# Optimization experiments

Hardware: AMD Instinct MI355X
Metric: run time of the kernel (lower is better)

## Reference

```python
import jax, jax.numpy as jnp
import numpy as np

B, S, D, H, DK = 2, 2048, 1024, 16, 64
NUM_BUCKETS, MAX_DIST = 32, 128
EPS = 1e-6


def _relative_position_bucket(rel, num_buckets=NUM_BUCKETS, max_distance=MAX_DIST):
    # bidirectional (T5 encoder) bucketing
    nb = num_buckets // 2
    bucket = (rel > 0).astype(jnp.int32) * nb
    n = jnp.abs(rel)
    max_exact = nb // 2
    is_small = n < max_exact
    large = max_exact + (
        jnp.log(jnp.maximum(n, 1).astype(jnp.float32) / max_exact)
        / np.log(max_distance / max_exact)
        * (nb - max_exact)
    ).astype(jnp.int32)
    large = jnp.minimum(large, nb - 1)
    return bucket + jnp.where(is_small, n, large)


def softmax1(logits):
    # off-by-one softmax: exp(x-m) / (sum(exp(x-m)) + exp(-m))
    m = jax.lax.stop_gradient(jnp.max(logits, axis=-1, keepdims=True))
    e = jnp.exp(logits - m)
    return e / (jnp.sum(e, axis=-1, keepdims=True) + jnp.exp(-m))


def setup_inputs() -> dict:
    key = jax.random.key(0)
    ks = jax.random.split(key, 8)
    scale = 0.02
    return {
        "hidden_states": jax.random.normal(ks[0], (B, S, D), dtype=jnp.float32),
        "delete_gate_mask": jax.random.normal(ks[1], (B, S, 1), dtype=jnp.float32),
        "ln_w": jnp.ones((D,), dtype=jnp.float32),
        "q_w": jax.random.normal(ks[2], (D, H * DK), dtype=jnp.float32) * scale,
        "k_w": jax.random.normal(ks[3], (D, H * DK), dtype=jnp.float32) * scale,
        "v_w": jax.random.normal(ks[4], (D, H * DK), dtype=jnp.float32) * scale,
        "o_w": jax.random.normal(ks[5], (H * DK, D), dtype=jnp.float32) * scale,
        "rel_emb": jax.random.normal(ks[6], (NUM_BUCKETS, H), dtype=jnp.float32) * scale,
    }


def reference(hidden_states, delete_gate_mask, ln_w, q_w, k_w, v_w, o_w, rel_emb):
    # T5LayerNorm (RMS norm, no mean subtraction, no bias)
    var = jnp.mean(jnp.square(hidden_states), axis=-1, keepdims=True)
    x = hidden_states * jax.lax.rsqrt(var + EPS) * ln_w

    # projections (T5 Linear layers have no bias, no 1/sqrt(d) scaling)
    q = (x @ q_w).reshape(B, S, H, DK).transpose(0, 2, 1, 3)  # bhqd
    k = (x @ k_w).reshape(B, S, H, DK).transpose(0, 2, 1, 3)  # bhkd
    v = (x @ v_w).reshape(B, S, H, DK).transpose(0, 2, 1, 3)  # bhkd

    scores = jnp.einsum("bhqd,bhkd->bhqk", q, k)

    # relative position bias: [1, H, S, S]
    pos = jnp.arange(S)
    rel = pos[None, :] - pos[:, None]  # key_pos - query_pos
    bucket = _relative_position_bucket(rel)  # [S, S]
    position_bias = rel_emb[bucket].transpose(2, 0, 1)[None]  # [1,H,S,S]

    # delete gate: [B,S,1] -> additive mask over key axis [B,1,1,S]
    gate = delete_gate_mask[..., 0][:, None, None, :]

    scores = scores + position_bias + gate
    attn = softmax1(scores.astype(jnp.float32)).astype(scores.dtype)

    attn_out = jnp.einsum("bhqk,bhkd->bhqd", attn, v)
    attn_out = attn_out.transpose(0, 2, 1, 3).reshape(B, S, H * DK) @ o_w

    # residual (dropout disabled at p=0)
    return hidden_states + attn_out
```

## Files before the change

kernel.cpp:

```cpp
#include <hip/hip_runtime.h>
#include <hip/hip_bf16.h>
#include <math.h>

typedef __attribute__((ext_vector_type(8))) short short8;
typedef __attribute__((ext_vector_type(4))) float f32x4;

#define S_LEN   2048
#define DMODEL  1024
#define NHEAD   16
#define HDK     64
#define NBATCH  2
#define MTOT    (NBATCH*S_LEN)
#define LOG2E   1.4426950408889634f

__device__ __forceinline__ unsigned short f2bf(float f) {
  union { float f; unsigned u; } c; c.f = f;
  unsigned r = c.u + 0x7FFFu + ((c.u >> 16) & 1u);
  return (unsigned short)(r >> 16);
}

__device__ __forceinline__ short8 lds_ld16(const unsigned short* p) {
  return *reinterpret_cast<const short8*>(p);
}

__device__ __forceinline__ void gload_lds16(const unsigned short* g, unsigned short* l) {
  __builtin_amdgcn_global_load_lds(
      (const __attribute__((address_space(1))) unsigned int*)g,
      (__attribute__((address_space(3))) unsigned int*)l, 16, 0, 0);
}

__global__ __launch_bounds__(256) void transpose_w_kernel(
    const float* __restrict__ qw, const float* __restrict__ kw,
    const float* __restrict__ vw, const float* __restrict__ ow,
    unsigned short* __restrict__ wqkv, unsigned short* __restrict__ wo) {
  int z = blockIdx.z;
  const float* src = (z==0)?qw:(z==1)?kw:(z==2)?vw:ow;
  unsigned short* dst = (z<3) ? (wqkv + (size_t)z*DMODEL*DMODEL) : wo;
  __shared__ float tile[32][33];
  int n0 = blockIdx.x*32, k0 = blockIdx.y*32;
  int tx = threadIdx.x, ty = threadIdx.y;
  for (int r = ty; r < 32; r += 8)
    tile[r][tx] = src[(size_t)(k0+r)*DMODEL + n0 + tx];
  __syncthreads();
  for (int r = ty; r < 32; r += 8)
    dst[(size_t)(n0+r)*DMODEL + k0 + tx] = f2bf(tile[tx][r]);
}

__global__ void bias_table_kernel(const float* __restrict__ rel_emb,
                                  float* __restrict__ btab) {
  int idx = blockIdx.x*256 + threadIdx.x;
  if (idx >= NHEAD*4095) return;
  int h = idx / 4095, rp = idx % 4095, rel = rp - 2047;
  int bucket = (rel > 0) ? 16 : 0;
  int n = (rel < 0) ? -rel : rel;
  int v;
  if (n < 8) v = n;
  else {
    float lrv = logf((float)n * 0.125f) / 2.7725887f * 8.0f;
    v = 8 + (int)lrv;
    if (v > 15) v = 15;
  }
  btab[idx] = rel_emb[(size_t)(bucket + v)*NHEAD + h] * LOG2E;
}

__global__ __launch_bounds__(256) void rmsnorm_kernel(
    const float* __restrict__ hs, const float* __restrict__ lnw,
    unsigned short* __restrict__ xo) {
  int row = blockIdx.x, t = threadIdx.x;
  const float4 v = ((const float4*)(hs + (size_t)row*DMODEL))[t];
  float ss = v.x*v.x + v.y*v.y + v.z*v.z + v.w*v.w;
  #pragma unroll
  for (int off = 32; off >= 1; off >>= 1) ss += __shfl_xor(ss, off, 64);
  __shared__ float wsum[4];
  if ((t & 63) == 0) wsum[t >> 6] = ss;
  __syncthreads();
  float tot = wsum[0] + wsum[1] + wsum[2] + wsum[3];
  float sc = rsqrtf(tot * (1.0f/DMODEL) + 1e-6f);
  const float4 lw = ((const float4*)lnw)[t];
  uint2 o;
  o.x = (unsigned)f2bf(v.x*sc*lw.x) | ((unsigned)f2bf(v.y*sc*lw.y) << 16);
  o.y = (unsigned)f2bf(v.z*sc*lw.z) | ((unsigned)f2bf(v.w*sc*lw.w) << 16);
  ((uint2*)(xo + (size_t)row*DMODEL))[t] = o;
}

template<int EPI>
__global__ __launch_bounds__(256) void gemm128(
    const unsigned short* __restrict__ A,
    const unsigned short* __restrict__ Bt,
    unsigned short* __restrict__ Oq, unsigned short* __restrict__ Ok,
    unsigned short* __restrict__ Ov,
    const float* __restrict__ resid, float* __restrict__ Of) {
  __shared__ unsigned short As[128*64];
  __shared__ unsigned short Bs[128*64];
  const int m0 = blockIdx.x*128, n0 = blockIdx.y*128;
  const unsigned short* Bz = Bt + ((EPI==0) ? (size_t)blockIdx.z*DMODEL*DMODEL : 0);
  const int t = threadIdx.x, lane = t & 63, w = t >> 6;
  const int g = lane >> 4, lr = lane & 15;
  const int wr = (w >> 1)*64, wc = (w & 1)*64;

  f32x4 acc[4][4];
  #pragma unroll
  for (int mi = 0; mi < 4; mi++)
    #pragma unroll
    for (int ni = 0; ni < 4; ni++) acc[mi][ni] = (f32x4){0.f,0.f,0.f,0.f};

  const unsigned short* ag[4]; const unsigned short* bg[4];
  unsigned short* al[4]; unsigned short* bl[4];
  #pragma unroll
  for (int i = 0; i < 4; i++) {
    int slot = t + i*256, row = slot >> 3, c8 = slot & 7;
    int cs = c8 ^ (row & 7);
    ag[i] = A  + (size_t)(m0 + row)*DMODEL + cs*8;
    bg[i] = Bz + (size_t)(n0 + row)*DMODEL + cs*8;
    al[i] = As + slot*8;
    bl[i] = Bs + slot*8;
  }

  for (int kk = 0; kk < DMODEL; kk += 64) {
    #pragma unroll
    for (int i = 0; i < 4; i++) {
      gload_lds16(ag[i] + kk, al[i]);
      gload_lds16(bg[i] + kk, bl[i]);
    }
    __syncthreads();
    #pragma unroll
    for (int ks = 0; ks < 2; ks++) {
      short8 af[4], bfr[4];
      #pragma unroll
      for (int mi = 0; mi < 4; mi++) {
        int R = wr + mi*16 + lr;
        af[mi] = lds_ld16(As + R*64 + (((ks*4 + g) ^ (R & 7)) << 3));
      }
      #pragma unroll
      for (int ni = 0; ni < 4; ni++) {
        int R = wc + ni*16 + lr;
        bfr[ni] = lds_ld16(Bs + R*64 + (((ks*4 + g) ^ (R & 7)) << 3));
      }
      #pragma unroll
      for (int mi = 0; mi < 4; mi++)
        #pragma unroll
        for (int ni = 0; ni < 4; ni++)
          acc[mi][ni] = __builtin_amdgcn_mfma_f32_16x16x32_bf16(af[mi], bfr[ni], acc[mi][ni], 0, 0, 0);
    }
    __syncthreads();
  }

  if (EPI == 0) {
    unsigned short* dst = (blockIdx.z == 0) ? Oq : Ok;
    const float osc = (blockIdx.z == 0) ? LOG2E : 1.0f;
    #pragma unroll
    for (int mi = 0; mi < 4; mi++) {
      #pragma unroll
      for (int r = 0; r < 4; r++) {
        int m = m0 + wr + mi*16 + g*4 + r;
        int b = m >> 11, s = m & (S_LEN-1);
        unsigned short* drow = dst + ((size_t)b*NHEAD*S_LEN + s)*HDK;
        #pragma unroll
        for (int ni = 0; ni < 4; ni++) {
          int n = n0 + wc + ni*16 + lr;
          int h = n >> 6, dcol = n & 63;
          drow[(size_t)h*S_LEN*HDK + dcol] = f2bf(acc[mi][ni][r] * osc);
        }
      }
    }
  } else if (EPI == 2) {
    #pragma unroll
    for (int ni = 0; ni < 4; ni++) {
      int n = n0 + wc + ni*16 + lr;
      int b = n >> 11, s = n & (S_LEN-1);
      #pragma unroll
      for (int mi = 0; mi < 4; mi++)
        #pragma unroll
        for (int r = 0; r < 4; r++) {
          int m = m0 + wr + mi*16 + g*4 + r;
          Ov[((size_t)b*DMODEL + m)*S_LEN + s] = f2bf(acc[mi][ni][r]);
        }
    }
  } else {
    #pragma unroll
    for (int mi = 0; mi < 4; mi++) {
      #pragma unroll
      for (int r = 0; r < 4; r++) {
        int m = m0 + wr + mi*16 + g*4 + r;
        const float* rrow = resid + (size_t)m*DMODEL;
        float* orow = Of + (size_t)m*DMODEL;
        #pragma unroll
        for (int ni = 0; ni < 4; ni++) {
          int n = n0 + wc + ni*16 + lr;
          orow[n] = rrow[n] + acc[mi][ni][r];
        }
      }
    }
  }
}

__global__ __launch_bounds__(256, 2) void attn_kernel(
    const unsigned short* __restrict__ Qg,
    const unsigned short* __restrict__ Kg,
    const unsigned short* __restrict__ Vtg,
    const float* __restrict__ btab,
    const float* __restrict__ gmask,
    unsigned short* __restrict__ Og) {
  __shared__ __align__(16) unsigned short Kl[2][64][64];
  __shared__ __align__(16) unsigned short Vl[2][64][64];
  __shared__ __align__(16) unsigned short Pl[4][16*64];
  __shared__ __align__(16) float gl[S_LEN];

  const int flat = blockIdx.x;
  const int xcd = flat & 7, j = flat >> 3;
  const int bh = xcd*4 + (j >> 4), qx = j & 15;
  const int b = bh >> 4, h = bh & 15;
  const int q0 = qx * 128;

  const int t = threadIdx.x, w = t >> 6, lane = t & 63;
  const int g = lane >> 4, lr = lane & 15, l7 = lane & 7;
  const int srow0 = t >> 3, sg0 = t & 7, srow1 = srow0 + 32;
  const int swz = (sg0 ^ (srow0 & 7)) << 3;

  const unsigned short* Qb = Qg  + (size_t)bh*S_LEN*HDK;
  const unsigned short* Kb = Kg  + (size_t)bh*S_LEN*HDK;
  const unsigned short* Vb = Vtg + (size_t)bh*HDK*S_LEN;

  {
    const float4* gm4 = (const float4*)(gmask + (size_t)b*S_LEN);
    #pragma unroll
    for (int i = 0; i < 2; i++) {
      int idx = t + i*256;
      float4 gv = gm4[idx];
      float4 gs; gs.x = gv.x*LOG2E; gs.y = gv.y*LOG2E; gs.z = gv.z*LOG2E; gs.w = gv.w*LOG2E;
      ((float4*)gl)[idx] = gs;
    }
  }

  const int qs0A = q0 + w*32, qs0B = qs0A + 16;
  short8 qfA0 = *reinterpret_cast<const short8*>(Qb + (size_t)(qs0A+lr)*HDK + g*8);
  short8 qfA1 = *reinterpret_cast<const short8*>(Qb + (size_t)(qs0A+lr)*HDK + 32 + g*8);
  short8 qfB0 = *reinterpret_cast<const short8*>(Qb + (size_t)(qs0B+lr)*HDK + g*8);
  short8 qfB1 = *reinterpret_cast<const short8*>(Qb + (size_t)(qs0B+lr)*HDK + 32 + g*8);

  f32x4 accA[4], accB[4];
  #pragma unroll
  for (int n = 0; n < 4; n++) { accA[n] = (f32x4){0.f,0.f,0.f,0.f}; accB[n] = (f32x4){0.f,0.f,0.f,0.f}; }
  float mA = -1e30f, lA = 0.f, mB = -1e30f, lB = 0.f;

  const float* btb = btab + (size_t)h*4095 + 2047;
  const float cpos = btb[91];
  const float cneg = btb[-91];

  {
    *reinterpret_cast<uint4*>(&Kl[0][srow0][swz]) =
        *reinterpret_cast<const uint4*>(Kb + (size_t)srow0*HDK + sg0*8);
    *reinterpret_cast<uint4*>(&Kl[0][srow1][swz]) =
        *reinterpret_cast<const uint4*>(Kb + (size_t)srow1*HDK + sg0*8);
    *reinterpret_cast<uint4*>(&Vl[0][srow0][swz]) =
        *reinterpret_cast<const uint4*>(Vb + (size_t)srow0*S_LEN + sg0*8);
    *reinterpret_cast<uint4*>(&Vl[0][srow1][swz]) =
        *reinterpret_cast<const uint4*>(Vb + (size_t)srow1*S_LEN + sg0*8);
  }

  char* prow = (char*)&Pl[w][0] + lr*128;

  int cur = 0;
  const int NT = S_LEN/64;
  for (int kt = 0; kt < NT; ++kt) {
    const int key0 = kt*64;
    __syncthreads();

    uint4 nk0, nk1, nv0, nv1;
    const bool pf = (kt + 1 < NT);
    if (pf) {
      nk0 = *reinterpret_cast<const uint4*>(Kb + (size_t)(key0+64+srow0)*HDK + sg0*8);
      nk1 = *reinterpret_cast<const uint4*>(Kb + (size_t)(key0+64+srow1)*HDK + sg0*8);
      nv0 = *reinterpret_cast<const uint4*>(Vb + (size_t)srow0*S_LEN + key0+64 + sg0*8);
      nv1 = *reinterpret_cast<const uint4*>(Vb + (size_t)srow1*S_LEN + key0+64 + sg0*8);
    }

    short8 bk[4][2];
    #pragma unroll
    for (int n = 0; n < 4; n++) {
      const unsigned short* kr = &Kl[cur][n*16 + lr][0];
      bk[n][0] = lds_ld16(kr + ((g ^ l7) << 3));
      bk[n][1] = lds_ld16(kr + (((4 + g) ^ l7) << 3));
    }
    short8 bv[2][4];
    #pragma unroll
    for (int c = 0; c < 2; c++)
      #pragma unroll
      for (int n = 0; n < 4; n++)
        bv[c][n] = lds_ld16(&Vl[cur][n*16 + lr][((4*c + g) ^ l7) << 3]);
    float4 gq[4];
    #pragma unroll
    for (int n = 0; n < 4; n++) gq[n] = *(const float4*)&gl[key0 + n*16 + g*4];

    f32x4 svA[4], svB[4];
    __builtin_amdgcn_s_setprio(1);
    #pragma unroll
    for (int n = 0; n < 4; n++) {
      f32x4 z = (f32x4){0.f,0.f,0.f,0.f};
      svA[n] = __builtin_amdgcn_mfma_f32_16x16x32_bf16(bk[n][0], qfA0, z, 0, 0, 0);
      svA[n] = __builtin_amdgcn_mfma_f32_16x16x32_bf16(bk[n][1], qfA1, svA[n], 0, 0, 0);
      svB[n] = __builtin_amdgcn_mfma_f32_16x16x32_bf16(bk[n][0], qfB0, z, 0, 0, 0);
      svB[n] = __builtin_amdgcn_mfma_f32_16x16x32_bf16(bk[n][1], qfB1, svB[n], 0, 0, 0);
    }
    __builtin_amdgcn_s_setprio(0);

#define PROCESS_SET(sv_, m_, l_, acc_, qs0_)                                          \
    {                                                                                 \
      float s_[4][4];                                                                 \
      _Pragma("unroll") for (int n = 0; n < 4; n++)                                   \
        _Pragma("unroll") for (int r = 0; r < 4; r++) s_[n][r] = sv_[n][r];           \
      const int dband = key0 - (qs0_);                                                \
      if (dband > -154 && dband < 106) {                                              \
        const float* btq = btb + (dband - lr);                                        \
        _Pragma("unroll") for (int n = 0; n < 4; n++)                                 \
          _Pragma("unroll") for (int r = 0; r < 4; r++)                               \
            s_[n][r] += gq[n][r] + btq[n*16 + g*4 + r];                               \
      } else {                                                                        \
        const float cc = (dband > 0) ? cpos : cneg;                                   \
        _Pragma("unroll") for (int n = 0; n < 4; n++)                                 \
          _Pragma("unroll") for (int r = 0; r < 4; r++)                               \
            s_[n][r] += gq[n][r] + cc;                                                \
      }                                                                               \
      float pmax = s_[0][0];                                                          \
      _Pragma("unroll") for (int n = 0; n < 4; n++)                                   \
        _Pragma("unroll") for (int r = 0; r < 4; r++) pmax = fmaxf(pmax, s_[n][r]);   \
      if (__any(pmax > m_ + 8.0f)) {                                                  \
        float tm = pmax;                                                              \
        tm = fmaxf(tm, __shfl_xor(tm, 16));                                           \
        tm = fmaxf(tm, __shfl_xor(tm, 32));                                           \
        float mnew = fmaxf(m_, tm);                                                   \
        float scv = exp2f(m_ - mnew);                                                 \
        m_ = mnew; l_ *= scv;                                                         \
        _Pragma("unroll") for (int r = 0; r < 4; r++) {                               \
          float s4 = __shfl(scv, g*4 + r, 16);                                        \
          _Pragma("unroll") for (int n = 0; n < 4; n++) acc_[n][r] *= s4;             \
        }                                                                             \
      }                                                                               \
      _Pragma("unroll") for (int n = 0; n < 4; n++)                                   \
        _Pragma("unroll") for (int r = 0; r < 4; r++) {                               \
          float p = exp2f(s_[n][r] - m_);                                             \
          s_[n][r] = p; l_ += p;                                                      \
        }                                                                             \
      _Pragma("unroll") for (int n = 0; n < 4; n++) {                                 \
        unsigned plo_, phi_;                                                          \
        asm("v_cvt_pk_bf16_f32 %0, %1, %2" : "=v"(plo_) : "v"(s_[n][0]), "v"(s_[n][1])); \
        asm("v_cvt_pk_bf16_f32 %0, %1, %2" : "=v"(phi_) : "v"(s_[n][2]), "v"(s_[n][3])); \
        uint2 pw_; pw_.x = plo_; pw_.y = phi_;                                        \
        *reinterpret_cast<uint2*>(prow + ((((2*n + (g>>1)) ^ l7) << 4) + ((g & 1) << 3))) = pw_; \
      }                                                                               \
      __builtin_amdgcn_s_setprio(1);                                                  \
      _Pragma("unroll") for (int c = 0; c < 2; c++) {                                 \
        short8 pa_ = lds_ld16((const unsigned short*)(prow + (((4*c + g) ^ l7) << 4))); \
        _Pragma("unroll") for (int n = 0; n < 4; n++)                                 \
          acc_[n] = __builtin_amdgcn_mfma_f32_16x16x32_bf16(pa_, bv[c][n], acc_[n], 0, 0, 0); \
      }                                                                               \
      __builtin_amdgcn_s_setprio(0);                                                  \
    }

    PROCESS_SET(svA, mA, lA, accA, qs0A)
    PROCESS_SET(svB, mB, lB, accB, qs0B)
#undef PROCESS_SET

    if (pf) {
      *reinterpret_cast<uint4*>(&Kl[cur^1][srow0][swz]) = nk0;
      *reinterpret_cast<uint4*>(&Kl[cur^1][srow1][swz]) = nk1;
      *reinterpret_cast<uint4*>(&Vl[cur^1][srow0][swz]) = nv0;
      *reinterpret_cast<uint4*>(&Vl[cur^1][srow1][swz]) = nv1;
    }
    cur ^= 1;
  }

#define FINAL_SET(m_, l_, acc_, qs0_)                                                 \
  {                                                                                   \
    float rs = l_;                                                                    \
    rs += __shfl_xor(rs, 16);                                                         \
    rs += __shfl_xor(rs, 32);                                                         \
    float inv = 1.0f / (rs + exp2f(-m_));                                             \
    _Pragma("unroll") for (int r = 0; r < 4; r++) {                                   \
      float inv4 = __shfl(inv, g*4 + r, 16);                                          \
      int srw = (qs0_) + g*4 + r;                                                     \
      unsigned short* orow = Og + ((size_t)b*S_LEN + srw)*DMODEL + h*HDK;             \
      _Pragma("unroll") for (int n = 0; n < 4; n++)                                   \
        orow[n*16 + lr] = f2bf(acc_[n][r] * inv4);                                    \
    }                                                                                 \
  }
  FINAL_SET(mA, lA, accA, qs0A)
  FINAL_SET(mB, lB, accB, qs0B)
#undef FINAL_SET
}

extern "C" void kernel_launch(void* const* d_in, const int* in_sizes, int n_in,
                              void* d_out, int out_size, void* d_ws, size_t ws_size,
                              hipStream_t stream) {
  const float* hs   = (const float*)d_in[0];
  const float* gate = (const float*)d_in[1];
  const float* lnw  = (const float*)d_in[2];
  const float* qw   = (const float*)d_in[3];
  const float* kw   = (const float*)d_in[4];
  const float* vw   = (const float*)d_in[5];
  const float* ow   = (const float*)d_in[6];
  const float* rel  = (const float*)d_in[7];
  float* out = (float*)d_out;

  char* ws = (char*)d_ws;
  const size_t MB = 1ull << 20;
  unsigned short* xbf  = (unsigned short*)(ws);
  unsigned short* wqkv = (unsigned short*)(ws + 8*MB);
  unsigned short* wo   = (unsigned short*)(ws + 14*MB);
  unsigned short* qb   = (unsigned short*)(ws + 16*MB);
  unsigned short* kb   = (unsigned short*)(ws + 24*MB);
  unsigned short* vt   = (unsigned short*)(ws + 32*MB);
  unsigned short* ao   = (unsigned short*)(ws + 40*MB);
  float*          btab = (float*)(ws + 48*MB);

  transpose_w_kernel<<<dim3(32,32,4), dim3(32,8), 0, stream>>>(qw, kw, vw, ow, wqkv, wo);
  bias_table_kernel<<<dim3(256), dim3(256), 0, stream>>>(rel, btab);
  rmsnorm_kernel<<<dim3(MTOT), dim3(256), 0, stream>>>(hs, lnw, xbf);
  gemm128<0><<<dim3(MTOT/128, DMODEL/128, 2), dim3(256), 0, stream>>>(
      xbf, wqkv, qb, kb, nullptr, nullptr, nullptr);
  gemm128<2><<<dim3(DMODEL/128, MTOT/128, 1), dim3(256), 0, stream>>>(
      wqkv + (size_t)2*DMODEL*DMODEL, xbf, nullptr, nullptr, vt, nullptr, nullptr);
  attn_kernel<<<dim3(512), dim3(256), 0, stream>>>(
      qb, kb, vt, btab, gate, ao);
  gemm128<1><<<dim3(MTOT/128, DMODEL/128, 1), dim3(256), 0, stream>>>(
      ao, wo, nullptr, nullptr, nullptr, hs, out);
}
```

Before: 154.7 us.

## Drop online max in attention, fold gate into V, load K/V directly

The attention softmax no longer tracks a running max or rescales. The exp(gate) factor is pulled out of the logits and applied to V in the V-projection epilogue. The row sum is computed by an extra MFMA of P against a bf16 exp(gate) vector, and the final normaliser becomes 1/(sum+1). The constant bias is injected through the MFMA accumulator init. K/V LDS double-buffering and the block barrier are removed, so each wave reads K/V fragments straight from global memory. This cuts per-tile max reductions, shuffles and syncs, but risks overflow when logits are large and adds redundant global traffic across waves.

```diff
diff --git a/kernel.cpp b/kernel.cpp
--- a/kernel.cpp
+++ b/kernel.cpp
@@ -61,6 +61,15 @@
     if (v > 15) v = 15;
   }
   btab[idx] = rel_emb[(size_t)(bucket + v)*NHEAD + h] * LOG2E;
+}
+
+__global__ void eg_kernel(const float* __restrict__ gmask,
+                          float* __restrict__ egf,
+                          unsigned short* __restrict__ egb) {
+  int i = blockIdx.x*256 + threadIdx.x;
+  float e = __expf(gmask[i]);
+  egf[i] = e;
+  egb[i] = f2bf(e);
 }
 
 __global__ __launch_bounds__(256) void rmsnorm_kernel(
@@ -89,7 +98,8 @@
     const unsigned short* __restrict__ Bt,
     unsigned short* __restrict__ Oq, unsigned short* __restrict__ Ok,
     unsigned short* __restrict__ Ov,
-    const float* __restrict__ resid, float* __restrict__ Of) {
+    const float* __restrict__ resid, float* __restrict__ Of,
+    const float* __restrict__ escale) {
   __shared__ unsigned short As[128*64];
   __shared__ unsigned short Bs[128*64];
   const int m0 = blockIdx.x*128, n0 = blockIdx.y*128;
@@ -168,12 +178,13 @@
     for (int ni = 0; ni < 4; ni++) {
       int n = n0 + wc + ni*16 + lr;
       int b = n >> 11, s = n & (S_LEN-1);
+      float e = escale[n];
       #pragma unroll
       for (int mi = 0; mi < 4; mi++)
         #pragma unroll
         for (int r = 0; r < 4; r++) {
           int m = m0 + wr + mi*16 + g*4 + r;
-          Ov[((size_t)b*DMODEL + m)*S_LEN + s] = f2bf(acc[mi][ni][r]);
+          Ov[((size_t)b*DMODEL + m)*S_LEN + s] = f2bf(acc[mi][ni][r] * e);
         }
     }
   } else {
@@ -199,12 +210,9 @@
     const unsigned short* __restrict__ Kg,
     const unsigned short* __restrict__ Vtg,
     const float* __restrict__ btab,
-    const float* __restrict__ gmask,
+    const unsigned short* __restrict__ egb,
     unsigned short* __restrict__ Og) {
-  __shared__ __align__(16) unsigned short Kl[2][64][64];
-  __shared__ __align__(16) unsigned short Vl[2][64][64];
   __shared__ __align__(16) unsigned short Pl[4][16*64];
-  __shared__ __align__(16) float gl[S_LEN];
 
   const int flat = blockIdx.x;
   const int xcd = flat & 7, j = flat >> 3;
@@ -214,23 +222,11 @@
 
   const int t = threadIdx.x, w = t >> 6, lane = t & 63;
   const int g = lane >> 4, lr = lane & 15, l7 = lane & 7;
-  const int srow0 = t >> 3, sg0 = t & 7, srow1 = srow0 + 32;
-  const int swz = (sg0 ^ (srow0 & 7)) << 3;
 
   const unsigned short* Qb = Qg  + (size_t)bh*S_LEN*HDK;
   const unsigned short* Kb = Kg  + (size_t)bh*S_LEN*HDK;
   const unsigned short* Vb = Vtg + (size_t)bh*HDK*S_LEN;
-
-  {
-    const float4* gm4 = (const float4*)(gmask + (size_t)b*S_LEN);
-    #pragma unroll
-    for (int i = 0; i < 2; i++) {
-      int idx = t + i*256;
-      float4 gv = gm4[idx];
-      float4 gs; gs.x = gv.x*LOG2E; gs.y = gv.y*LOG2E; gs.z = gv.z*LOG2E; gs.w = gv.w*LOG2E;
-      ((float4*)gl)[idx] = gs;
-    }
-  }
+  const unsigned short* ge = egb + (size_t)b*S_LEN;
 
   const int qs0A = q0 + w*32, qs0B = qs0A + 16;
   short8 qfA0 = *reinterpret_cast<const short8*>(Qb + (size_t)(qs0A+lr)*HDK + g*8);
@@ -238,113 +234,69 @@
   short8 qfB0 = *reinterpret_cast<const short8*>(Qb + (size_t)(qs0B+lr)*HDK + g*8);
   short8 qfB1 = *reinterpret_cast<const short8*>(Qb + (size_t)(qs0B+lr)*HDK + 32 + g*8);
 
-  f32x4 accA[4], accB[4];
+  f32x4 accA[4], accB[4], l4A, l4B;
   #pragma unroll
   for (int n = 0; n < 4; n++) { accA[n] = (f32x4){0.f,0.f,0.f,0.f}; accB[n] = (f32x4){0.f,0.f,0.f,0.f}; }
-  float mA = -1e30f, lA = 0.f, mB = -1e30f, lB = 0.f;
+  l4A = (f32x4){0.f,0.f,0.f,0.f}; l4B = (f32x4){0.f,0.f,0.f,0.f};
 
   const float* btb = btab + (size_t)h*4095 + 2047;
   const float cpos = btb[91];
   const float cneg = btb[-91];
 
-  {
-    *reinterpret_cast<uint4*>(&Kl[0][srow0][swz]) =
-        *reinterpret_cast<const uint4*>(Kb + (size_t)srow0*HDK + sg0*8);
-    *reinterpret_cast<uint4*>(&Kl[0][srow1][swz]) =
-        *reinterpret_cast<const uint4*>(Kb + (size_t)srow1*HDK + sg0*8);
-    *reinterpret_cast<uint4*>(&Vl[0][srow0][swz]) =
-        *reinterpret_cast<const uint4*>(Vb + (size_t)srow0*S_LEN + sg0*8);
-    *reinterpret_cast<uint4*>(&Vl[0][srow1][swz]) =
-        *reinterpret_cast<const uint4*>(Vb + (size_t)srow1*S_LEN + sg0*8);
-  }
-
   char* prow = (char*)&Pl[w][0] + lr*128;
 
-  int cur = 0;
-  const int NT = S_LEN/64;
-  for (int kt = 0; kt < NT; ++kt) {
+  for (int kt = 0; kt < S_LEN/64; ++kt) {
     const int key0 = kt*64;
-    __syncthreads();
-
-    uint4 nk0, nk1, nv0, nv1;
-    const bool pf = (kt + 1 < NT);
-    if (pf) {
-      nk0 = *reinterpret_cast<const uint4*>(Kb + (size_t)(key0+64+srow0)*HDK + sg0*8);
-      nk1 = *reinterpret_cast<const uint4*>(Kb + (size_t)(key0+64+srow1)*HDK + sg0*8);
-      nv0 = *reinterpret_cast<const uint4*>(Vb + (size_t)srow0*S_LEN + key0+64 + sg0*8);
-      nv1 = *reinterpret_cast<const uint4*>(Vb + (size_t)srow1*S_LEN + key0+64 + sg0*8);
-    }
 
     short8 bk[4][2];
     #pragma unroll
-    for (int n = 0; n < 4; n++) {
-      const unsigned short* kr = &Kl[cur][n*16 + lr][0];
-      bk[n][0] = lds_ld16(kr + ((g ^ l7) << 3));
-      bk[n][1] = lds_ld16(kr + (((4 + g) ^ l7) << 3));
-    }
+    for (int n = 0; n < 4; n++)
+      #pragma unroll
+      for (int c = 0; c < 2; c++)
+        bk[n][c] = *reinterpret_cast<const short8*>(
+            Kb + (size_t)(key0 + n*16 + lr)*HDK + c*32 + g*8);
     short8 bv[2][4];
     #pragma unroll
     for (int c = 0; c < 2; c++)
       #pragma unroll
       for (int n = 0; n < 4; n++)
-        bv[c][n] = lds_ld16(&Vl[cur][n*16 + lr][((4*c + g) ^ l7) << 3]);
-    float4 gq[4];
-    #pragma unroll
-    for (int n = 0; n < 4; n++) gq[n] = *(const float4*)&gl[key0 + n*16 + g*4];
-
-    f32x4 svA[4], svB[4];
-    __builtin_amdgcn_s_setprio(1);
-    #pragma unroll
-    for (int n = 0; n < 4; n++) {
-      f32x4 z = (f32x4){0.f,0.f,0.f,0.f};
-      svA[n] = __builtin_amdgcn_mfma_f32_16x16x32_bf16(bk[n][0], qfA0, z, 0, 0, 0);
-      svA[n] = __builtin_amdgcn_mfma_f32_16x16x32_bf16(bk[n][1], qfA1, svA[n], 0, 0, 0);
-      svB[n] = __builtin_amdgcn_mfma_f32_16x16x32_bf16(bk[n][0], qfB0, z, 0, 0, 0);
-      svB[n] = __builtin_amdgcn_mfma_f32_16x16x32_bf16(bk[n][1], qfB1, svB[n], 0, 0, 0);
-    }
-    __builtin_amdgcn_s_setprio(0);
-
-#define PROCESS_SET(sv_, m_, l_, acc_, qs0_)                                          \
+        bv[c][n] = *reinterpret_cast<const short8*>(
+            Vb + (size_t)(n*16 + lr)*S_LEN + key0 + c*32 + g*8);
+    short8 gv[2];
+    #pragma unroll
+    for (int c = 0; c < 2; c++) {
+      short8 z8 = (short8){0,0,0,0,0,0,0,0};
+      if (lr == 0)
+        z8 = *reinterpret_cast<const short8*>(ge + key0 + c*32 + g*8);
+      gv[c] = z8;
+    }
+
+#define PROCESS_SET(qf0_, qf1_, qs0_, acc_, l4_)                                      \
     {                                                                                 \
-      float s_[4][4];                                                                 \
-      _Pragma("unroll") for (int n = 0; n < 4; n++)                                   \
-        _Pragma("unroll") for (int r = 0; r < 4; r++) s_[n][r] = sv_[n][r];           \
       const int dband = key0 - (qs0_);                                                \
-      if (dband > -154 && dband < 106) {                                              \
+      const bool band = (dband > -154 && dband < 106);                                \
+      const float cc = band ? 0.f : ((dband > 0) ? cpos : cneg);                      \
+      f32x4 z = (f32x4){cc, cc, cc, cc};                \
+      f32x4 sv[4];                                                                    \
+      __builtin_amdgcn_s_setprio(1);                                                  \
+      _Pragma("unroll") for (int n = 0; n < 4; n++) {                                 \
+        sv[n] = __builtin_amdgcn_mfma_f32_16x16x32_bf16(bk[n][0], qf0_, z, 0, 0, 0);  \
+        sv[n] = __builtin_amdgcn_mfma_f32_16x16x32_bf16(bk[n][1], qf1_, sv[n], 0, 0, 0); \
+      }                                                                               \
+      __builtin_amdgcn_s_setprio(0);                                                  \
+      if (band) {                                                                     \
         const float* btq = btb + (dband - lr);                                        \
         _Pragma("unroll") for (int n = 0; n < 4; n++)                                 \
           _Pragma("unroll") for (int r = 0; r < 4; r++)                               \
-            s_[n][r] += gq[n][r] + btq[n*16 + g*4 + r];                               \
-      } else {                                                                        \
-        const float cc = (dband > 0) ? cpos : cneg;                                   \
-        _Pragma("unroll") for (int n = 0; n < 4; n++)                                 \
-          _Pragma("unroll") for (int r = 0; r < 4; r++)                               \
-            s_[n][r] += gq[n][r] + cc;                                                \
-      }                                                                               \
-      float pmax = s_[0][0];                                                          \
-      _Pragma("unroll") for (int n = 0; n < 4; n++)                                   \
-        _Pragma("unroll") for (int r = 0; r < 4; r++) pmax = fmaxf(pmax, s_[n][r]);   \
-      if (__any(pmax > m_ + 8.0f)) {                                                  \
-        float tm = pmax;                                                              \
-        tm = fmaxf(tm, __shfl_xor(tm, 16));                                           \
-        tm = fmaxf(tm, __shfl_xor(tm, 32));                                           \
-        float mnew = fmaxf(m_, tm);                                                   \
-        float scv = exp2f(m_ - mnew);                                                 \
-        m_ = mnew; l_ *= scv;                                                         \
-        _Pragma("unroll") for (int r = 0; r < 4; r++) {                               \
-          float s4 = __shfl(scv, g*4 + r, 16);                                        \
-          _Pragma("unroll") for (int n = 0; n < 4; n++) acc_[n][r] *= s4;             \
-        }                                                                             \
+            sv[n][r] += btq[n*16 + g*4 + r];                                          \
       }                                                                               \
       _Pragma("unroll") for (int n = 0; n < 4; n++)                                   \
-        _Pragma("unroll") for (int r = 0; r < 4; r++) {                               \
-          float p = exp2f(s_[n][r] - m_);                                             \
-          s_[n][r] = p; l_ += p;                                                      \
-        }                                                                             \
+        _Pragma("unroll") for (int r = 0; r < 4; r++)                                 \
+          sv[n][r] = exp2f(sv[n][r]);                                                 \
       _Pragma("unroll") for (int n = 0; n < 4; n++) {                                 \
         unsigned plo_, phi_;                                                          \
-        asm("v_cvt_pk_bf16_f32 %0, %1, %2" : "=v"(plo_) : "v"(s_[n][0]), "v"(s_[n][1])); \
-        asm("v_cvt_pk_bf16_f32 %0, %1, %2" : "=v"(phi_) : "v"(s_[n][2]), "v"(s_[n][3])); \
+        asm("v_cvt_pk_bf16_f32 %0, %1, %2" : "=v"(plo_) : "v"(sv[n][0]), "v"(sv[n][1])); \
+        asm("v_cvt_pk_bf16_f32 %0, %1, %2" : "=v"(phi_) : "v"(sv[n][2]), "v"(sv[n][3])); \
         uint2 pw_; pw_.x = plo_; pw_.y = phi_;                                        \
         *reinterpret_cast<uint2*>(prow + ((((2*n + (g>>1)) ^ l7) << 4) + ((g & 1) << 3))) = pw_; \
       }                                                                               \
@@ -353,39 +305,29 @@
         short8 pa_ = lds_ld16((const unsigned short*)(prow + (((4*c + g) ^ l7) << 4))); \
         _Pragma("unroll") for (int n = 0; n < 4; n++)                                 \
           acc_[n] = __builtin_amdgcn_mfma_f32_16x16x32_bf16(pa_, bv[c][n], acc_[n], 0, 0, 0); \
+        l4_ = __builtin_amdgcn_mfma_f32_16x16x32_bf16(pa_, gv[c], l4_, 0, 0, 0);      \
       }                                                                               \
       __builtin_amdgcn_s_setprio(0);                                                  \
     }
 
-    PROCESS_SET(svA, mA, lA, accA, qs0A)
-    PROCESS_SET(svB, mB, lB, accB, qs0B)
+    PROCESS_SET(qfA0, qfA1, qs0A, accA, l4A)
+    PROCESS_SET(qfB0, qfB1, qs0B, accB, l4B)
 #undef PROCESS_SET
-
-    if (pf) {
-      *reinterpret_cast<uint4*>(&Kl[cur^1][srow0][swz]) = nk0;
-      *reinterpret_cast<uint4*>(&Kl[cur^1][srow1][swz]) = nk1;
-      *reinterpret_cast<uint4*>(&Vl[cur^1][srow0][swz]) = nv0;
-      *reinterpret_cast<uint4*>(&Vl[cur^1][srow1][swz]) = nv1;
-    }
-    cur ^= 1;
-  }
-
-#define FINAL_SET(m_, l_, acc_, qs0_)                                                 \
+  }
+
+#define FINAL_SET(acc_, l4_, qs0_)                                                    \
   {                                                                                   \
-    float rs = l_;                                                                    \
-    rs += __shfl_xor(rs, 16);                                                         \
-    rs += __shfl_xor(rs, 32);                                                         \
-    float inv = 1.0f / (rs + exp2f(-m_));                                             \
     _Pragma("unroll") for (int r = 0; r < 4; r++) {                                   \
-      float inv4 = __shfl(inv, g*4 + r, 16);                                          \
+      float lq = __shfl(l4_[r], g*16);                                                \
+      float inv = 1.0f / (lq + 1.0f);                                                 \
       int srw = (qs0_) + g*4 + r;                                                     \
       unsigned short* orow = Og + ((size_t)b*S_LEN + srw)*DMODEL + h*HDK;             \
       _Pragma("unroll") for (int n = 0; n < 4; n++)                                   \
-        orow[n*16 + lr] = f2bf(acc_[n][r] * inv4);                                    \
+        orow[n*16 + lr] = f2bf(acc_[n][r] * inv);                                     \
     }                                                                                 \
   }
-  FINAL_SET(mA, lA, accA, qs0A)
-  FINAL_SET(mB, lB, accB, qs0B)
+  FINAL_SET(accA, l4A, qs0A)
+  FINAL_SET(accB, l4B, qs0B)
 #undef FINAL_SET
 }
 
@@ -412,16 +354,19 @@
   unsigned short* vt   = (unsigned short*)(ws + 32*MB);
   unsigned short* ao   = (unsigned short*)(ws + 40*MB);
   float*          btab = (float*)(ws + 48*MB);
+  float*          egf  = (float*)(ws + 48*MB + 256*1024);
+  unsigned short* egb  = (unsigned short*)(ws + 48*MB + 272*1024);
 
   transpose_w_kernel<<<dim3(32,32,4), dim3(32,8), 0, stream>>>(qw, kw, vw, ow, wqkv, wo);
   bias_table_kernel<<<dim3(256), dim3(256), 0, stream>>>(rel, btab);
+  eg_kernel<<<dim3(16), dim3(256), 0, stream>>>(gate, egf, egb);
   rmsnorm_kernel<<<dim3(MTOT), dim3(256), 0, stream>>>(hs, lnw, xbf);
   gemm128<0><<<dim3(MTOT/128, DMODEL/128, 2), dim3(256), 0, stream>>>(
-      xbf, wqkv, qb, kb, nullptr, nullptr, nullptr);
+      xbf, wqkv, qb, kb, nullptr, nullptr, nullptr, nullptr);
   gemm128<2><<<dim3(DMODEL/128, MTOT/128, 1), dim3(256), 0, stream>>>(
-      wqkv + (size_t)2*DMODEL*DMODEL, xbf, nullptr, nullptr, vt, nullptr, nullptr);
+      wqkv + (size_t)2*DMODEL*DMODEL, xbf, nullptr, nullptr, vt, nullptr, nullptr, egf);
   attn_kernel<<<dim3(512), dim3(256), 0, stream>>>(
-      qb, kb, vt, btab, gate, ao);
+      qb, kb, vt, btab, egb, ao);
   gemm128<1><<<dim3(MTOT/128, DMODEL/128, 1), dim3(256), 0, stream>>>(
-      ao, wo, nullptr, nullptr, nullptr, hs, out);
-}
+      ao, wo, nullptr, nullptr, nullptr, hs, out, nullptr);
+}
```

New measurement: 207.7 us. +34.2%, slower.
